# Kernel tuning notes

Measured on AMD Instinct MI355X. Metric: run time of the kernel, lower is better.

## Reference

```python
import jax, jax.numpy as jnp
from jax import lax
import numpy as np

B, L, D_MODEL = 4, 2048, 1024
D_STATE, D_CONV, EXPAND = 16, 4, 2
D_INNER = EXPAND * D_MODEL          # 2048
DT_RANK = D_MODEL // 16             # 64
LN_EPS = 1e-5


def setup_inputs() -> dict:
    key = jax.random.key(0)
    ks = jax.random.split(key, 8)
    s = 0.02
    # S4D-real init for A_log, as in Mamba
    A_init = jnp.tile(jnp.arange(1, D_STATE + 1, dtype=jnp.float32), (D_INNER, 1))
    return {
        "x": jax.random.normal(ks[0], (B, L, D_MODEL), jnp.float32),
        "ln_g": jnp.ones((D_MODEL,), jnp.float32),
        "ln_b": jnp.zeros((D_MODEL,), jnp.float32),
        "W_in": jax.random.normal(ks[1], (D_MODEL, 2 * D_INNER), jnp.float32) * s,
        "conv_w": jax.random.normal(ks[2], (D_INNER, D_CONV), jnp.float32) * s,
        "conv_b": jnp.zeros((D_INNER,), jnp.float32),
        "W_x": jax.random.normal(ks[3], (D_INNER, DT_RANK + 2 * D_STATE), jnp.float32) * s,
        "W_dt": jax.random.normal(ks[4], (DT_RANK, D_INNER), jnp.float32) * s,
        "b_dt": jnp.full((D_INNER,), -4.6, jnp.float32),  # softplus(b_dt) ~ 0.01
        "A_log": jnp.log(A_init),
        "Dskip": jnp.ones((D_INNER,), jnp.float32),
        "W_out": jax.random.normal(ks[5], (D_INNER, D_MODEL), jnp.float32) * s,
    }


def _layer_norm(x, g, b):
    mu = jnp.mean(x, -1, keepdims=True)
    var = jnp.mean((x - mu) ** 2, -1, keepdims=True)
    return (x - mu) * lax.rsqrt(var + LN_EPS) * g + b


def _mamba_block(x, ln_g, ln_b, W_in, conv_w, conv_b, W_x, W_dt, b_dt, A_log, Dskip, W_out):
    b, l, _ = x.shape
    xn = _layer_norm(x, ln_g, ln_b)

    # in_proj -> (u, z), each (B, L, d_inner)
    xz = xn @ W_in
    u, z = jnp.split(xz, 2, axis=-1)

    # causal depthwise conv over L + SiLU
    u_t = u.transpose(0, 2, 1)                      # (B, d_inner, L)
    k = conv_w[:, None, :]                          # (d_inner, 1, d_conv)
    uc = lax.conv_general_dilated(
        u_t, k, (1,), [(D_CONV - 1, 0)],
        dimension_numbers=("NCH", "OIH", "NCH"),
        feature_group_count=D_INNER,
    ) + conv_b[None, :, None]
    uc = jax.nn.silu(uc).transpose(0, 2, 1)         # (B, L, d_inner)

    # input-dependent dt, B, C
    dbc = uc @ W_x                                  # (B, L, dt_rank + 2*d_state)
    dt_r = dbc[..., :DT_RANK]
    Bs = dbc[..., DT_RANK:DT_RANK + D_STATE]        # (B, L, d_state)
    Cs = dbc[..., DT_RANK + D_STATE:]               # (B, L, d_state)
    dt = jax.nn.softplus(dt_r @ W_dt + b_dt)        # (B, L, d_inner)

    A = -jnp.exp(A_log)                             # (d_inner, d_state)

    def step(h, ins):
        dt_t, B_t, C_t, u_t = ins                   # (b,di),(b,ds),(b,ds),(b,di)
        dA = jnp.exp(dt_t[..., None] * A)           # (b, di, ds)
        h = h * dA + (dt_t * u_t)[..., None] * B_t[:, None, :]
        y = jnp.einsum("bds,bs->bd", h, C_t)
        return h, y

    h0 = jnp.zeros((b, D_INNER, D_STATE), x.dtype)
    xs = (dt.transpose(1, 0, 2), Bs.transpose(1, 0, 2),
          Cs.transpose(1, 0, 2), uc.transpose(1, 0, 2))
    _, ys = lax.scan(step, h0, xs)                  # (L, B, d_inner)
    y = ys.transpose(1, 0, 2) + uc * Dskip          # D skip connection
    y = y * jax.nn.silu(z)                          # gate
    return x + y @ W_out                            # residual (dropout=0)


def reference(x, ln_g, ln_b, W_in, conv_w, conv_b, W_x, W_dt, b_dt, A_log, Dskip, W_out):
    return _mamba_block(x, ln_g, ln_b, W_in, conv_w, conv_b, W_x, W_dt, b_dt, A_log, Dskip, W_out)
```

## Files before the change

### kernel.cpp

```cpp
#include <hip/hip_runtime.h>
#include <hip/hip_bf16.h>

#define BB 4
#define LL 2048
#define DM 1024
#define DI 2048
#define DST 16
#define DTR 64
#define ROWS (BB*LL)
#define NC 32
#define CHUNK (LL/NC)

using bf16x8 = __attribute__((ext_vector_type(8))) __bf16;
using f32x4  = __attribute__((ext_vector_type(4))) float;

#define AS1 __attribute__((address_space(1)))
#define AS3 __attribute__((address_space(3)))

__global__ __launch_bounds__(256) void transpose_all_kernel(
        const float* __restrict__ Wi, const float* __restrict__ Wo,
        const float* __restrict__ Wx, const float* __restrict__ Wd,
        __hip_bfloat16* __restrict__ WiT, __hip_bfloat16* __restrict__ WoT,
        __hip_bfloat16* __restrict__ WxT, __hip_bfloat16* __restrict__ WdT) {
    const int t = blockIdx.x;
    const float* src; __hip_bfloat16* dst; int R, C, Cpad, nx, idx;
    if (t < 4096)      { src = Wi; dst = WiT; R = 1024; C = 4096; Cpad = 4096; nx = 128; idx = t; }
    else if (t < 6144) { src = Wo; dst = WoT; R = 2048; C = 1024; Cpad = 1024; nx = 32;  idx = t - 4096; }
    else if (t < 6400) { src = Wx; dst = WxT; R = 2048; C = 96;   Cpad = 128;  nx = 4;   idx = t - 6144; }
    else               { src = Wd; dst = WdT; R = 64;   C = 2048; Cpad = 2048; nx = 64;  idx = t - 6400; }
    __shared__ float tl[32][33];
    const int c0 = (idx % nx) * 32, r0 = (idx / nx) * 32;
    const int tx = threadIdx.x & 31, ty = threadIdx.x >> 5;
    #pragma unroll
    for (int k = 0; k < 4; k++) {
        const int r = r0 + ty + 8 * k, c = c0 + tx;
        tl[ty + 8 * k][tx] = (r < R && c < C) ? src[(size_t)r * C + c] : 0.f;
    }
    __syncthreads();
    #pragma unroll
    for (int k = 0; k < 4; k++) {
        const int c = c0 + ty + 8 * k, r = r0 + tx;
        if (c < Cpad && r < R) dst[(size_t)c * R + r] = __float2bfloat16(tl[tx][ty + 8 * k]);
    }
}

__global__ __launch_bounds__(256) void ln_bf16_kernel(const float* __restrict__ x,
                                                      const float* __restrict__ g,
                                                      const float* __restrict__ bta,
                                                      __hip_bfloat16* __restrict__ xn) {
    const int row = blockIdx.x;
    const int tid = threadIdx.x;
    const float4 v = ((const float4*)(x + (size_t)row * DM))[tid];
    float s  = v.x + v.y + v.z + v.w;
    float sq = v.x*v.x + v.y*v.y + v.z*v.z + v.w*v.w;
    #pragma unroll
    for (int m = 1; m < 64; m <<= 1) {
        s  += __shfl_xor(s, m);
        sq += __shfl_xor(sq, m);
    }
    __shared__ float ss[4], ssq[4];
    const int w = tid >> 6;
    if ((tid & 63) == 0) { ss[w] = s; ssq[w] = sq; }
    __syncthreads();
    s  = ss[0] + ss[1] + ss[2] + ss[3];
    sq = ssq[0] + ssq[1] + ssq[2] + ssq[3];
    const float mu  = s * (1.f / DM);
    const float var = sq * (1.f / DM) - mu * mu;
    const float rs  = rsqrtf(var + 1e-5f);
    const float4 gv = ((const float4*)g)[tid];
    const float4 bv = ((const float4*)bta)[tid];
    __hip_bfloat16* op = xn + (size_t)row * DM + tid * 4;
    op[0] = __float2bfloat16((v.x - mu) * rs * gv.x + bv.x);
    op[1] = __float2bfloat16((v.y - mu) * rs * gv.y + bv.y);
    op[2] = __float2bfloat16((v.z - mu) * rs * gv.z + bv.z);
    op[3] = __float2bfloat16((v.w - mu) * rs * gv.w + bv.w);
}

template<int MODE>
__global__ __launch_bounds__(256) void mfma_gemm(const __hip_bfloat16* __restrict__ A,
                                                 const __hip_bfloat16* __restrict__ Bt,
                                                 float* __restrict__ O,
                                                 __hip_bfloat16* __restrict__ Oz,
                                                 __hip_bfloat16* __restrict__ Ozb,
                                                 const float* __restrict__ Add,
                                                 int Kstride, int klen) {
    __shared__ __hip_bfloat16 As[2 * 128 * 32];
    __shared__ __hip_bfloat16 Bs[2 * 128 * 32];
    const int tid  = threadIdx.x;
    const int lane = tid & 63;
    const int w    = tid >> 6;

    const int nbx = gridDim.x, nby = gridDim.y;
    const int lid = blockIdx.y * nbx + blockIdx.x;
    const int rpx = nby >> 3;
    const int xcd = lid & 7, sl = lid >> 3;
    const int by  = xcd * rpx + (sl % rpx);
    const int bx  = sl / rpx;

    const int row0 = by * 128, col0 = bx * 128;
    const int wr0 = (w >> 1) * 64, wc0 = (w & 1) * 64;

    f32x4 acc[4][4];
    #pragma unroll
    for (int i = 0; i < 4; i++)
        #pragma unroll
        for (int j = 0; j < 4; j++) acc[i][j] = f32x4{0.f, 0.f, 0.f, 0.f};

    const int fm  = lane & 15;
    const int fqi = lane >> 4;
    const int fqX = ((fqi ^ (fm & 3)) << 3);

    const int kbeg = blockIdx.z * klen;
    for (int k0 = kbeg; k0 < kbeg + klen; k0 += 64) {
        #pragma unroll
        for (int j = 0; j < 4; j++) {
            const int c   = w * 256 + j * 64 + lane;
            const int p   = c >> 9;
            const int row = (c >> 2) & 127;
            const int q   = (c & 3) ^ (row & 3);
            const int gk  = k0 + p * 32 + q * 8;
            __builtin_amdgcn_global_load_lds(
                (const AS1 unsigned int*)(A + (size_t)(row0 + row) * Kstride + gk),
                (AS3 unsigned int*)(As + c * 8), 16, 0, 0);
            __builtin_amdgcn_global_load_lds(
                (const AS1 unsigned int*)(Bt + (size_t)(col0 + row) * Kstride + gk),
                (AS3 unsigned int*)(Bs + c * 8), 16, 0, 0);
        }
        __syncthreads();
        #pragma unroll
        for (int half = 0; half < 2; half++) {
            bf16x8 af[4], bfr[4];
            #pragma unroll
            for (int i = 0; i < 4; i++)
                af[i] = *(const bf16x8*)&As[half * 4096 + (wr0 + i * 16 + fm) * 32 + fqX];
            #pragma unroll
            for (int j = 0; j < 4; j++)
                bfr[j] = *(const bf16x8*)&Bs[half * 4096 + (wc0 + j * 16 + fm) * 32 + fqX];
            #pragma unroll
            for (int i = 0; i < 4; i++)
                #pragma unroll
                for (int j = 0; j < 4; j++)
                    acc[i][j] = __builtin_amdgcn_mfma_f32_16x16x32_bf16(af[i], bfr[j], acc[i][j], 0, 0, 0);
        }
        __syncthreads();
    }

    #pragma unroll
    for (int i = 0; i < 4; i++) {
        #pragma unroll
        for (int j = 0; j < 4; j++) {
            #pragma unroll
            for (int r = 0; r < 4; r++) {
                const int row = row0 + wr0 + i * 16 + (lane >> 4) * 4 + r;
                const int col = col0 + wc0 + j * 16 + fm;
                const float v = acc[i][j][r];
                if (MODE == 2) {
                    O[(size_t)row * DM + col] = v + Add[(size_t)row * DM + col];
                } else if (MODE == 3) {
                    const float t  = v + Add[col];
                    const float sp = (t > 20.f) ? t : __logf(1.f + __expf(t));
                    Oz[(size_t)row * DI + col] = __float2bfloat16(sp);
                } else if (MODE == 4) {
                    O[((size_t)blockIdx.z * ROWS + row) * 128 + col] = v;
                }
            }
        }
    }
}

#define STAGE_A(buf, half, kt) do {                                              \
    _Pragma("unroll")                                                            \
    for (int j_ = 0; j_ < 2; j_++) {                                             \
        const int strip_ = w * 2 + j_;                                           \
        __builtin_amdgcn_global_load_lds(                                        \
            (const AS1 unsigned int*)(A + (size_t)(row0 + (half)*128 + strip_*8 + srow) * Kstride + ((kt)*64 + schk*8)), \
            (AS3 unsigned int*)(&As[buf][half][strip_*8][0] + sldo), 16, 0, 0);  \
    } } while (0)

#define STAGE_B(buf, half, kt) do {                                              \
    _Pragma("unroll")                                                            \
    for (int j_ = 0; j_ < 2; j_++) {                                             \
        const int strip_ = w * 2 + j_;                                           \
        __builtin_amdgcn_global_load_lds(                                        \
            (const AS1 unsigned int*)(Bt + (size_t)(col0 + (half)*128 + strip_*8 + srow) * Kstride + ((kt)*64 + schk*8)), \
            (AS3 unsigned int*)(&Bs[buf][half][strip_*8][0] + sldo), 16, 0, 0);  \
    } } while (0)

#define LOAD_A(buf, MH) do {                                                     \
    _Pragma("unroll")                                                            \
    for (int i_ = 0; i_ < 4; i_++) {                                             \
        const int r_ = (MH)*64 + i_*16 + fm;                                     \
        a_[i_][0] = *(const bf16x8*)&As[buf][wm][r_][((fq    ) ^ (fm & 7)) << 3];\
        a_[i_][1] = *(const bf16x8*)&As[buf][wm][r_][((fq + 4) ^ (fm & 7)) << 3];\
    } } while (0)

#define LOAD_B(dst, buf, NP) do {                                                \
    _Pragma("unroll")                                                            \
    for (int j_ = 0; j_ < 2; j_++) {                                             \
        const int c_ = (wn & 1)*64 + (NP)*32 + j_*16 + fm;                       \
        dst[j_][0] = *(const bf16x8*)&Bs[buf][wn >> 1][c_][((fq    ) ^ (fm & 7)) << 3]; \
        dst[j_][1] = *(const bf16x8*)&Bs[buf][wn >> 1][c_][((fq + 4) ^ (fm & 7)) << 3]; \
    } } while (0)

#define MFMA_Q(MH, NP, bset) do {                                                \
    __builtin_amdgcn_s_setprio(1);                                               \
    _Pragma("unroll")                                                            \
    for (int i_ = 0; i_ < 4; i_++)                                               \
        _Pragma("unroll")                                                        \
        for (int j_ = 0; j_ < 2; j_++) {                                         \
            acc[(MH)*4+i_][(NP)*2+j_] = __builtin_amdgcn_mfma_f32_16x16x32_bf16( \
                a_[i_][0], bset[j_][0], acc[(MH)*4+i_][(NP)*2+j_], 0, 0, 0);     \
            acc[(MH)*4+i_][(NP)*2+j_] = __builtin_amdgcn_mfma_f32_16x16x32_bf16( \
                a_[i_][1], bset[j_][1], acc[(MH)*4+i_][(NP)*2+j_], 0, 0, 0);     \
        }                                                                        \
    __builtin_amdgcn_s_setprio(0);                                               \
} while (0)

#define PH_SYNC() do {                                                           \
    __builtin_amdgcn_s_barrier();                                                \
    asm volatile("s_waitcnt lgkmcnt(0)" ::: "memory");                           \
} while (0)

template<int MODE>
__global__ __launch_bounds__(512, 2) void mfma_gemm256(
        const __hip_bfloat16* __restrict__ A,
        const __hip_bfloat16* __restrict__ Bt,
        float* __restrict__ O,
        __hip_bfloat16* __restrict__ Oz,
        __hip_bfloat16* __restrict__ Ozb,
        const float* __restrict__ Add,
        int Kstride, int K) {
    __shared__ __hip_bfloat16 As[2][2][128][64];
    __shared__ __hip_bfloat16 Bs[2][2][128][64];
    const int tid  = threadIdx.x;
    const int lane = tid & 63;
    const int w    = tid >> 6;
    const int wm   = w >> 2;
    const int wn   = w & 3;
    const int fm   = lane & 15;
    const int fq   = lane >> 4;

    const int nbx = gridDim.x, nby = gridDim.y;
    const int lid = blockIdx.y * nbx + blockIdx.x;
    const int rpx = nby >> 3;
    const int xcd = lid & 7, sl = lid >> 3;
    const int by  = xcd * rpx + (sl % rpx);
    const int bx  = sl / rpx;
    const int row0 = by * 256, col0 = bx * 256;

    const int srow = lane >> 3;
    const int schk = (lane & 7) ^ srow;
    const int sldo = lane * 8;

    f32x4 acc[8][4];
    #pragma unroll
    for (int i = 0; i < 8; i++)
        #pragma unroll
        for (int j = 0; j < 4; j++) acc[i][j] = f32x4{0.f, 0.f, 0.f, 0.f};

    bf16x8 a_[4][2], b0_[2][2], b1_[2][2];

    STAGE_A(0, 0, 0); STAGE_A(0, 1, 0); STAGE_B(0, 0, 0); STAGE_B(0, 1, 0);
    STAGE_A(1, 0, 1); STAGE_A(1, 1, 1); STAGE_B(1, 0, 1);
    asm volatile("s_waitcnt vmcnt(6)" ::: "memory");
    __builtin_amdgcn_s_barrier();

    const int nt = K >> 6;
    for (int t = 0; t < nt; ++t) {
        const int buf = t & 1, ob = buf ^ 1;
        LOAD_A(buf, 0);
        LOAD_B(b0_, buf, 0);
        if (t + 1 < nt) STAGE_B(ob, 1, t + 1);
        PH_SYNC();
        MFMA_Q(0, 0, b0_);
        __builtin_amdgcn_s_barrier();
        LOAD_B(b1_, buf, 1);
        PH_SYNC();
        MFMA_Q(0, 1, b1_);
        __builtin_amdgcn_s_barrier();
        LOAD_A(buf, 1);
        if (t + 2 < nt) STAGE_B(buf, 0, t + 2);
        PH_SYNC();
        MFMA_Q(1, 1, b1_);
        __builtin_amdgcn_s_barrier();
        if (t + 2 < nt) {
            STAGE_A(buf, 0, t + 2); STAGE_A(buf, 1, t + 2);
            asm volatile("s_waitcnt vmcnt(6)" ::: "memory");
        } else {
            asm volatile("s_waitcnt vmcnt(0)" ::: "memory");
        }
        __builtin_amdgcn_s_barrier();
        MFMA_Q(1, 0, b0_);
        __builtin_amdgcn_s_barrier();
    }

    #pragma unroll
    for (int i = 0; i < 8; i++) {
        #pragma unroll
        for (int j = 0; j < 4; j++) {
            #pragma unroll
            for (int r = 0; r < 4; r++) {
                const int row = row0 + wm * 128 + i * 16 + fq * 4 + r;
                const int col = col0 + wn * 64 + j * 16 + fm;
                const float v = acc[i][j][r];
                if (MODE == 0) {
                    if (col0 < DI) Oz[(size_t)row * DI + col] = __float2bfloat16(v);
                    else           Ozb[(size_t)row * DI + (col - DI)] = __float2bfloat16(v);
                } else if (MODE == 2) {
                    O[(size_t)row * DM + col] = v + Add[(size_t)row * DM + col];
                }
            }
        }
    }
}
#undef STAGE_A
#undef STAGE_B
#undef LOAD_A
#undef LOAD_B
#undef MFMA_Q
#undef PH_SYNC

__global__ __launch_bounds__(256) void dbc_reduce_kernel(const float* __restrict__ pbuf,
                                                         float* __restrict__ dbc,
                                                         __hip_bfloat16* __restrict__ dbc64) {
    const size_t gid = (size_t)blockIdx.x * 256 + threadIdx.x;
    const int    col = gid & 127;
    const size_t row = gid >> 7;
    float sum = 0.f;
    #pragma unroll
    for (int sp = 0; sp < 4; sp++)
        sum += pbuf[((size_t)sp * ROWS + row) * 128 + col];
    if (col < DTR)                   dbc64[row * DTR + col] = __float2bfloat16(sum);
    else if (col < DTR + 2 * DST)    dbc[row * 128 + col] = sum;
}

__global__ __launch_bounds__(256) void conv_silu_kernel(const __hip_bfloat16* __restrict__ u,
                                                        const float* __restrict__ cw,
                                                        const float* __restrict__ cb,
                                                        __hip_bfloat16* __restrict__ uc) {
    const int d  = blockIdx.x * 256 + threadIdx.x;
    const int b  = blockIdx.z;
    const int l0 = blockIdx.y * 16;
    const float w0 = cw[d * 4 + 0], w1 = cw[d * 4 + 1];
    const float w2 = cw[d * 4 + 2], w3 = cw[d * 4 + 3];
    const float bias = cb[d];
    const __hip_bfloat16* up = u + (size_t)(b * LL) * DI + d;
    float x0 = (l0 - 3 >= 0) ? __bfloat162float(up[(size_t)(l0 - 3) * DI]) : 0.f;
    float x1 = (l0 - 2 >= 0) ? __bfloat162float(up[(size_t)(l0 - 2) * DI]) : 0.f;
    float x2 = (l0 - 1 >= 0) ? __bfloat162float(up[(size_t)(l0 - 1) * DI]) : 0.f;
    __hip_bfloat16* op = uc + (size_t)(b * LL + l0) * DI + d;
    #pragma unroll
    for (int i = 0; i < 16; i++) {
        const float x3 = __bfloat162float(up[(size_t)(l0 + i) * DI]);
        const float v  = bias + w0 * x0 + w1 * x1 + w2 * x2 + w3 * x3;
        const float sig = __builtin_amdgcn_rcpf(1.f + __expf(-v));
        op[(size_t)i * DI] = __float2bfloat16(v * sig);
        x0 = x1; x1 = x2; x2 = x3;
    }
}

__global__ __launch_bounds__(256) void scan_pass1_kernel(const __hip_bfloat16* __restrict__ dtb,
                                                         const __hip_bfloat16* __restrict__ uc,
                                                         const float* __restrict__ dbc,
                                                         const float* __restrict__ A_log,
                                                         float* __restrict__ hbuf,
                                                         float* __restrict__ Pbuf) {
    __shared__ float Bsh[CHUNK][16];
    const int tid = threadIdx.x;
    const int d   = blockIdx.x * 256 + tid;
    const int c   = blockIdx.y;
    const int b   = blockIdx.z;
    const size_t row0 = (size_t)b * LL + (size_t)c * CHUNK;

    {
        const int r = tid >> 2, j4 = (tid & 3) * 4;
        *(float4*)&Bsh[r][j4] = *(const float4*)(dbc + (row0 + r) * 128 + DTR + j4);
    }
    float a[DST];
    #pragma unroll
    for (int q = 0; q < 4; q++) {
        const float4 t = *(const float4*)(A_log + (size_t)d * DST + q * 4);
        a[q * 4 + 0] = -__expf(t.x); a[q * 4 + 1] = -__expf(t.y);
        a[q * 4 + 2] = -__expf(t.z); a[q * 4 + 3] = -__expf(t.w);
    }
    __syncthreads();

    const __hip_bfloat16* dtp = dtb + row0 * DI + d;
    const __hip_bfloat16* ucp = uc + row0 * DI + d;

    float h[DST];
    #pragma unroll
    for (int s = 0; s < DST; s++) h[s] = 0.f;
    float sdt = 0.f;
    float dtv = __bfloat162float(dtp[0]), ucv = __bfloat162float(ucp[0]);
    for (int l = 0; l < CHUNK; l++) {
        const int ln = (l + 1 < CHUNK) ? (l + 1) : l;
        const float dtn = __bfloat162float(dtp[(size_t)ln * DI]);
        const float ucn = __bfloat162float(ucp[(size_t)ln * DI]);
        const float dtu = dtv * ucv;
        sdt += dtv;
        #pragma unroll
        for (int s = 0; s < DST; s++) {
            const float dA = __expf(dtv * a[s]);
            h[s] = fmaf(h[s], dA, dtu * Bsh[l][s]);
        }
        dtv = dtn; ucv = ucn;
    }
    float* hp = hbuf + (((size_t)b * NC + c) * DI + d) * DST;
    float* pp = Pbuf + (((size_t)b * NC + c) * DI + d) * DST;
    #pragma unroll
    for (int q = 0; q < 4; q++) {
        *(float4*)&hp[q * 4] = float4{h[q*4+0], h[q*4+1], h[q*4+2], h[q*4+3]};
        *(float4*)&pp[q * 4] = float4{__expf(sdt * a[q*4+0]), __expf(sdt * a[q*4+1]),
                                      __expf(sdt * a[q*4+2]), __expf(sdt * a[q*4+3])};
    }
}

__global__ __launch_bounds__(256) void scan_combine_kernel(float* __restrict__ hbuf,
                                                           const float* __restrict__ Pbuf) {
    const size_t gid  = (size_t)blockIdx.x * 256 + threadIdx.x;
    const size_t b    = gid >> 15;
    const size_t d16s = gid & 32767;
    float H = 0.f;
    #pragma unroll
    for (int c = 0; c < NC; c++) {
        const size_t idx = (b * NC + c) * (DI * DST) + d16s;
        const float hc = hbuf[idx];
        const float Pc = Pbuf[idx];
        hbuf[idx] = H;
        H = hc + Pc * H;
    }
}

__global__ __launch_bounds__(256) void scan_pass3_kernel(const __hip_bfloat16* __restrict__ dtb,
                                                         __hip_bfloat16* uc,
                                                         const __hip_bfloat16* __restrict__ z,
                                                         const float* __restrict__ dbc,
                                                         const float* __restrict__ A_log,
                                                         const float* __restrict__ Dskip,
                                                         const float* __restrict__ hbuf) {
    __shared__ float BC[CHUNK][32];
    const int tid = threadIdx.x;
    const int d   = blockIdx.x * 256 + tid;
    const int c   = blockIdx.y;
    const int b   = blockIdx.z;
    const size_t row0 = (size_t)b * LL + (size_t)c * CHUNK;

    #pragma unroll
    for (int i = 0; i < 2; i++) {
        const int idx = i * 256 + tid;
        const int r = idx >> 3, j4 = (idx & 7) * 4;
        *(float4*)&BC[r][j4] = *(const float4*)(dbc + (row0 + r) * 128 + DTR + j4);
    }
    float a[DST];
    #pragma unroll
    for (int q = 0; q < 4; q++) {
        const float4 t = *(const float4*)(A_log + (size_t)d * DST + q * 4);
        a[q * 4 + 0] = -__expf(t.x); a[q * 4 + 1] = -__expf(t.y);
        a[q * 4 + 2] = -__expf(t.z); a[q * 4 + 3] = -__expf(t.w);
    }
    const float dsk = Dskip[d];
    __syncthreads();

    const __hip_bfloat16* dtp = dtb + row0 * DI + d;
    __hip_bfloat16* ucp = uc + row0 * DI + d;
    const __hip_bfloat16* zp = z + row0 * DI + d;

    float h[DST];
    {
        const float* hp = hbuf + (((size_t)b * NC + c) * DI + d) * DST;
        #pragma unroll
        for (int q = 0; q < 4; q++) {
            const float4 t = *(const float4*)&hp[q * 4];
            h[q*4+0] = t.x; h[q*4+1] = t.y; h[q*4+2] = t.z; h[q*4+3] = t.w;
        }
    }
    float dtv = __bfloat162float(dtp[0]);
    float ucv = __bfloat162float(ucp[0]);
    float zv  = __bfloat162float(zp[0]);
    for (int l = 0; l < CHUNK; l++) {
        const int ln = (l + 1 < CHUNK) ? (l + 1) : l;
        const float dtn = __bfloat162float(dtp[(size_t)ln * DI]);
        const float ucn = __bfloat162float(ucp[(size_t)ln * DI]);
        const float zn  = __bfloat162float(zp[(size_t)ln * DI]);
        const float dtu = dtv * ucv;
        float y = 0.f;
        #pragma unroll
        for (int s = 0; s < DST; s++) {
            const float dA = __expf(dtv * a[s]);
            h[s] = fmaf(h[s], dA, dtu * BC[l][s]);
            y = fmaf(h[s], BC[l][16 + s], y);
        }
        const float yt  = fmaf(ucv, dsk, y);
        const float sig = __builtin_amdgcn_rcpf(1.f + __expf(-zv));
        ucp[(size_t)l * DI] = __float2bfloat16(yt * (zv * sig));
        dtv = dtn; ucv = ucn; zv = zn;
    }
}

extern "C" void kernel_launch(void* const* d_in, const int* in_sizes, int n_in,
                              void* d_out, int out_size, void* d_ws, size_t ws_size,
                              hipStream_t stream) {
    const float* x      = (const float*)d_in[0];
    const float* ln_g   = (const float*)d_in[1];
    const float* ln_b   = (const float*)d_in[2];
    const float* W_in   = (const float*)d_in[3];
    const float* conv_w = (const float*)d_in[4];
    const float* conv_b = (const float*)d_in[5];
    const float* W_x    = (const float*)d_in[6];
    const float* W_dt   = (const float*)d_in[7];
    const float* b_dt   = (const float*)d_in[8];
    const float* A_log  = (const float*)d_in[9];
    const float* Dskip  = (const float*)d_in[10];
    const float* W_out  = (const float*)d_in[11];
    float* out = (float*)d_out;

    const size_t MB = 1024ull * 1024ull;
    char* wsb = (char*)d_ws;
    __hip_bfloat16* ub    = (__hip_bfloat16*)(wsb);
    __hip_bfloat16* z     = (__hip_bfloat16*)(wsb + 32 * MB);
    __hip_bfloat16* uc    = (__hip_bfloat16*)(wsb + 64 * MB);
    __hip_bfloat16* xn    = (__hip_bfloat16*)(wsb + 96 * MB);
    __hip_bfloat16* WinT  = (__hip_bfloat16*)(wsb + 112 * MB);
    __hip_bfloat16* WoutT = (__hip_bfloat16*)(wsb + 120 * MB);
    __hip_bfloat16* WxT   = (__hip_bfloat16*)(wsb + 124 * MB);
    float*          dbc   = (float*)(wsb + 125 * MB);
    float*          hbuf  = (float*)(wsb + 129 * MB);
    float*          Pbuf  = (float*)(wsb + 145 * MB);
    __hip_bfloat16* dbc64 = (__hip_bfloat16*)(wsb + 161 * MB);
    __hip_bfloat16* WdtT  = (__hip_bfloat16*)(wsb + 162 * MB);
    float*          pbuf  = (float*)(wsb + 163 * MB);
    __hip_bfloat16* dtb   = ub;

    transpose_all_kernel<<<6528, 256, 0, stream>>>(W_in, W_out, W_x, W_dt,
                                                   WinT, WoutT, WxT, WdtT);
    ln_bf16_kernel<<<ROWS, 256, 0, stream>>>(x, ln_g, ln_b, xn);
    mfma_gemm256<0><<<dim3(16, 32), 512, 0, stream>>>(
        xn, WinT, nullptr, ub, z, nullptr, DM, DM);
    conv_silu_kernel<<<dim3(DI / 256, LL / 16, BB), 256, 0, stream>>>(ub, conv_w, conv_b, uc);
    mfma_gemm<4><<<dim3(1, 64, 4), 256, 0, stream>>>(
        uc, WxT, pbuf, nullptr, nullptr, nullptr, DI, DI / 4);
    dbc_reduce_kernel<<<(ROWS * 128) / 256, 256, 0, stream>>>(pbuf, dbc, dbc64);
    mfma_gemm<3><<<dim3(DI / 128, ROWS / 128), 256, 0, stream>>>(
        dbc64, WdtT, nullptr, dtb, nullptr, b_dt, DTR, DTR);
    scan_pass1_kernel<<<dim3(DI / 256, NC, BB), 256, 0, stream>>>(dtb, uc, dbc, A_log, hbuf, Pbuf);
    scan_combine_kernel<<<(BB * DI * DST) / 256, 256, 0, stream>>>(hbuf, Pbuf);
    scan_pass3_kernel<<<dim3(DI / 256, NC, BB), 256, 0, stream>>>(dtb, uc, z, dbc, A_log, Dskip, hbuf);
    mfma_gemm<2><<<dim3(DM / 128, ROWS / 128), 256, 0, stream>>>(
        uc, WoutT, out, nullptr, nullptr, x, DI, DI);
}
```

Measured before the change: 430.8 us.

## Double-buffer A fragments and reschedule LDS reads to overlap MFMA in GEMM

Splits the A register fragments into two sets so the next tile's A half can be read from LDS while the current MFMAs run, and prefetches the first A fragments before the loop. The explicit lgkmcnt waits are removed, along with two of the per-iteration barriers. The aim is to hide LDS read latency behind MFMA work and cut synchronisation, at the cost of more VGPRs under launch_bounds(512,2). Without explicit waits, correctness relies on the compiler inserting the LDS waits, and the early LOAD_A on the other buffer may race with in-flight staging.

```diff
diff --git a/kernel.cpp b/kernel.cpp
--- a/kernel.cpp
+++ b/kernel.cpp
@@ -186,12 +186,20 @@
             (AS3 unsigned int*)(&Bs[buf][half][strip_*8][0] + sldo), 16, 0, 0);  \
     } } while (0)
 
-#define LOAD_A(buf, MH) do {                                                     \
+#define LOAD_A(dst, buf, MH) do {                                                \
     _Pragma("unroll")                                                            \
     for (int i_ = 0; i_ < 4; i_++) {                                             \
         const int r_ = (MH)*64 + i_*16 + fm;                                     \
-        a_[i_][0] = *(const bf16x8*)&As[buf][wm][r_][((fq    ) ^ (fm & 7)) << 3];\
-        a_[i_][1] = *(const bf16x8*)&As[buf][wm][r_][((fq + 4) ^ (fm & 7)) << 3];\
+        dst[i_][0] = *(const bf16x8*)&As[buf][wm][r_][((fq    ) ^ (fm & 7)) << 3];\
+        dst[i_][1] = *(const bf16x8*)&As[buf][wm][r_][((fq + 4) ^ (fm & 7)) << 3];\
+    } } while (0)
+
+#define LOAD_A_H(dst, buf, MH, P) do {                                           \
+    _Pragma("unroll")                                                            \
+    for (int i_ = (P)*2; i_ < (P)*2 + 2; i_++) {                                 \
+        const int r_ = (MH)*64 + i_*16 + fm;                                     \
+        dst[i_][0] = *(const bf16x8*)&As[buf][wm][r_][((fq    ) ^ (fm & 7)) << 3];\
+        dst[i_][1] = *(const bf16x8*)&As[buf][wm][r_][((fq + 4) ^ (fm & 7)) << 3];\
     } } while (0)
 
 #define LOAD_B(dst, buf, NP) do {                                                \
@@ -202,23 +210,18 @@
         dst[j_][1] = *(const bf16x8*)&Bs[buf][wn >> 1][c_][((fq + 4) ^ (fm & 7)) << 3]; \
     } } while (0)
 
-#define MFMA_Q(MH, NP, bset) do {                                                \
+#define MFMA_Q(aset, MH, NP, bset) do {                                          \
     __builtin_amdgcn_s_setprio(1);                                               \
     _Pragma("unroll")                                                            \
     for (int i_ = 0; i_ < 4; i_++)                                               \
         _Pragma("unroll")                                                        \
         for (int j_ = 0; j_ < 2; j_++) {                                         \
             acc[(MH)*4+i_][(NP)*2+j_] = __builtin_amdgcn_mfma_f32_16x16x32_bf16( \
-                a_[i_][0], bset[j_][0], acc[(MH)*4+i_][(NP)*2+j_], 0, 0, 0);     \
+                aset[i_][0], bset[j_][0], acc[(MH)*4+i_][(NP)*2+j_], 0, 0, 0);   \
             acc[(MH)*4+i_][(NP)*2+j_] = __builtin_amdgcn_mfma_f32_16x16x32_bf16( \
-                a_[i_][1], bset[j_][1], acc[(MH)*4+i_][(NP)*2+j_], 0, 0, 0);     \
+                aset[i_][1], bset[j_][1], acc[(MH)*4+i_][(NP)*2+j_], 0, 0, 0);   \
         }                                                                        \
     __builtin_amdgcn_s_setprio(0);                                               \
-} while (0)
-
-#define PH_SYNC() do {                                                           \
-    __builtin_amdgcn_s_barrier();                                                \
-    asm volatile("s_waitcnt lgkmcnt(0)" ::: "memory");                           \
 } while (0)
 
 template<int MODE>
@@ -258,30 +261,27 @@
         #pragma unroll
         for (int j = 0; j < 4; j++) acc[i][j] = f32x4{0.f, 0.f, 0.f, 0.f};
 
-    bf16x8 a_[4][2], b0_[2][2], b1_[2][2];
+    bf16x8 a0_[4][2], a1_[4][2], b0_[2][2], b1_[2][2];
 
     STAGE_A(0, 0, 0); STAGE_A(0, 1, 0); STAGE_B(0, 0, 0); STAGE_B(0, 1, 0);
     STAGE_A(1, 0, 1); STAGE_A(1, 1, 1); STAGE_B(1, 0, 1);
     asm volatile("s_waitcnt vmcnt(6)" ::: "memory");
     __builtin_amdgcn_s_barrier();
+    LOAD_A(a0_, 0, 0);
 
     const int nt = K >> 6;
     for (int t = 0; t < nt; ++t) {
         const int buf = t & 1, ob = buf ^ 1;
-        LOAD_A(buf, 0);
+        if (t + 1 < nt) STAGE_B(ob, 1, t + 1);
         LOAD_B(b0_, buf, 0);
-        if (t + 1 < nt) STAGE_B(ob, 1, t + 1);
-        PH_SYNC();
-        MFMA_Q(0, 0, b0_);
+        LOAD_B(b1_, buf, 1);
+        MFMA_Q(a0_, 0, 0, b0_);
+        LOAD_A_H(a1_, buf, 1, 0);
+        MFMA_Q(a0_, 0, 1, b1_);
         __builtin_amdgcn_s_barrier();
-        LOAD_B(b1_, buf, 1);
-        PH_SYNC();
-        MFMA_Q(0, 1, b1_);
-        __builtin_amdgcn_s_barrier();
-        LOAD_A(buf, 1);
         if (t + 2 < nt) STAGE_B(buf, 0, t + 2);
-        PH_SYNC();
-        MFMA_Q(1, 1, b1_);
+        LOAD_A_H(a1_, buf, 1, 1);
+        MFMA_Q(a1_, 1, 1, b1_);
         __builtin_amdgcn_s_barrier();
         if (t + 2 < nt) {
             STAGE_A(buf, 0, t + 2); STAGE_A(buf, 1, t + 2);
@@ -290,8 +290,8 @@
             asm volatile("s_waitcnt vmcnt(0)" ::: "memory");
         }
         __builtin_amdgcn_s_barrier();
-        MFMA_Q(1, 0, b0_);
-        __builtin_amdgcn_s_barrier();
+        if (t + 1 < nt) LOAD_A(a0_, ob, 0);
+        MFMA_Q(a1_, 1, 0, b0_);
     }
 
     #pragma unroll
@@ -316,9 +316,9 @@
 #undef STAGE_A
 #undef STAGE_B
 #undef LOAD_A
+#undef LOAD_A_H
 #undef LOAD_B
 #undef MFMA_Q
-#undef PH_SYNC
 
 __global__ __launch_bounds__(256) void dbc_reduce_kernel(const float* __restrict__ pbuf,
                                                          float* __restrict__ dbc,
```

New measurement: 436.4 us. No clear change (+1.3%).
